# Optimization experiments

Measured on AMD Instinct MI355X. Metric: run time of the kernel, lower is better.

The kernel has to match this reference:

```python
import jax, jax.numpy as jnp
import numpy as np

H = 12  # num_attention_heads

def setup_inputs() -> dict:
    key = jax.random.key(0)
    ks = jax.random.split(key, 6)
    B, S, D = 2, 2048, 768
    sc = 0.02
    return {
        "hidden_states": jax.random.normal(ks[0], (B, S, D), jnp.float32),
        "Wqr": jax.random.normal(ks[1], (D, D), jnp.float32) * sc,
        "Wqi": jax.random.normal(ks[2], (D, D), jnp.float32) * sc,
        "Wkr": jax.random.normal(ks[3], (D, D), jnp.float32) * sc,
        "Wki": jax.random.normal(ks[4], (D, D), jnp.float32) * sc,
        "Wv": jax.random.normal(ks[5], (D, D), jnp.float32) * sc,
    }

def _heads(x, B, S):
    # [B,S,D] -> [B,H,S,Dh]
    return x.reshape(B, S, H, -1).transpose(0, 2, 1, 3)

def reference(hidden_states, Wqr, Wqi, Wkr, Wki, Wv):
    B, S, D = hidden_states.shape
    Dh = D // H
    x = hidden_states  # real input; imag part is zero
    # complex projections with zero imag input: q = (x@Wqr.T) + i (x@Wqi.T), same for k
    qr = _heads(x @ Wqr.T, B, S)
    qi = _heads(x @ Wqi.T, B, S)
    kr = _heads(x @ Wkr.T, B, S)
    ki = _heads(x @ Wki.T, B, S)
    v = _heads(x @ Wv.T, B, S)
    scale = 1.0 / jnp.sqrt(jnp.float32(Dh))
    # complex QK^H in real arithmetic: s = q @ conj(k)^T
    sr = (jnp.einsum('bhqd,bhkd->bhqk', qr, kr) +
          jnp.einsum('bhqd,bhkd->bhqk', qi, ki)) * scale
    si = (jnp.einsum('bhqd,bhkd->bhqk', qi, kr) -
          jnp.einsum('bhqd,bhkd->bhqk', qr, ki)) * scale
    scores = jnp.sqrt(sr * sr + si * si)  # 'magnitude' variant
    probs = jax.nn.softmax(scores, axis=-1)
    ctx = jnp.einsum('bhqk,bhkd->bhqd', probs, v)
    return ctx.transpose(0, 2, 1, 3).reshape(B, S, D)
```

## Files before the change

kernel.cpp:

```cpp
#include <hip/hip_runtime.h>
#include <cstdint>

typedef short bf16x8 __attribute__((ext_vector_type(8)));
typedef float f32x4 __attribute__((ext_vector_type(4)));

#define MFMA16(a, b, c) __builtin_amdgcn_mfma_f32_16x16x32_bf16((a), (b), (c), 0, 0, 0)

__device__ __forceinline__ void gl16(const unsigned short* g, unsigned short* l) {
  __builtin_amdgcn_global_load_lds(
      (const __attribute__((address_space(1))) unsigned int*)g,
      (__attribute__((address_space(3))) unsigned int*)l, 16, 0, 0);
}

__device__ __forceinline__ unsigned short f2b(float f) {
  union { float f; unsigned int u; } x; x.f = f;
  unsigned int r = x.u + 0x7fffu + ((x.u >> 16) & 1u);
  return (unsigned short)(r >> 16);
}

__device__ __forceinline__ unsigned int pack2(float lo, float hi) {
  union { float f; unsigned int u; } a, b;
  a.f = lo; b.f = hi;
  return ((a.u + 0x8000u) >> 16) | ((b.u + 0x8000u) & 0xffff0000u);
}

#define NB 2
#define NS 2048
#define ND 768
#define NH 12
#define DHD 64
#define MTOK 4096

#define OFF_XB 0
#define OFF_WB 3145728
#define OFF_QK 6094848
#define OFF_VT 18677760

__global__ void cvt_kernel(const float* __restrict__ src,
                           unsigned short* __restrict__ dst, int n4, float scale) {
  int i = blockIdx.x * blockDim.x + threadIdx.x;
  if (i >= n4) return;
  float4 v = ((const float4*)src)[i];
  ushort4 o;
  o.x = f2b(v.x * scale); o.y = f2b(v.y * scale);
  o.z = f2b(v.z * scale); o.w = f2b(v.w * scale);
  ((ushort4*)dst)[i] = o;
}

__global__ void wcvt_kernel(const float* __restrict__ s0, const float* __restrict__ s1,
                            const float* __restrict__ s2, const float* __restrict__ s3,
                            const float* __restrict__ s4, unsigned short* __restrict__ dst,
                            float qs) {
  const int bz = blockIdx.x / 576;
  const int i = (blockIdx.x % 576) * 256 + threadIdx.x;
  const float* src = bz == 0 ? s0 : bz == 1 ? s1 : bz == 2 ? s2 : bz == 3 ? s3 : s4;
  const float scale = bz < 2 ? qs : 1.0f;
  float4 v = ((const float4*)src)[i];
  ushort4 o;
  o.x = f2b(v.x * scale); o.y = f2b(v.y * scale);
  o.z = f2b(v.z * scale); o.w = f2b(v.w * scale);
  ((ushort4*)(dst + bz * 589824))[i] = o;
}

__global__ __launch_bounds__(256) void proj_kernel(
    const unsigned short* __restrict__ Xb, const unsigned short* __restrict__ Wb,
    unsigned short* __restrict__ QK, unsigned short* __restrict__ Vt) {
  __shared__ __align__(16) unsigned short S[32768];

  const int lin = blockIdx.x + 6 * (blockIdx.y + 5 * blockIdx.z);
  const int sb = (lin & 7) * 120 + (lin >> 3);
  const int n0 = (sb % 6) * 128;
  const int rem = sb / 6;
  const int z = rem % 5;
  const int m0 = (rem / 5) * 128;

  const unsigned short* Wz = Wb + z * 589824;
  const int tid = threadIdx.x;
  const int lane = tid & 63;
  const int w = tid >> 6;
  const int wm = (w >> 1) * 64;
  const int wn = (w & 1) * 64;
  const int col = lane & 15, quad = lane >> 4;
  const int c7 = col & 7;

  const int lr = lane >> 3;
  const int lc = (lane & 7) ^ (lr & 7);
  const unsigned short* gX = Xb + (m0 + w * 32 + lr) * ND + lc * 8;
  const unsigned short* gW = Wz + (n0 + w * 32 + lr) * ND + lc * 8;
  unsigned short* lX = S + (w * 32) * 64;
  unsigned short* lW = S + 16384 + (w * 32) * 64;

  f32x4 acc[4][4] = {};

#pragma unroll
  for (int i = 0; i < 4; i++) {
    gl16(gX + i * (8 * ND), lX + i * 512);
    gl16(gW + i * (8 * ND), lW + i * 512);
  }
  __syncthreads();

  int cur = 0;
  for (int kk = 0; kk < 12; kk++) {
    if (kk < 11) {
      const int k0n = (kk + 1) * 64;
      unsigned short* dX = lX + ((cur ^ 1) * 8192);
      unsigned short* dW = lW + ((cur ^ 1) * 8192);
#pragma unroll
      for (int i = 0; i < 4; i++) {
        gl16(gX + i * (8 * ND) + k0n, dX + i * 512);
        gl16(gW + i * (8 * ND) + k0n, dW + i * 512);
      }
    }
    const unsigned short* Xc = S + cur * 8192;
    const unsigned short* Wc = S + 16384 + cur * 8192;
#pragma unroll
    for (int ks = 0; ks < 2; ks++) {
      bf16x8 af[4], bw[4];
#pragma unroll
      for (int t = 0; t < 4; t++) {
        const int fo = (((ks * 4 + quad) ^ c7) * 8);
        af[t] = *(const bf16x8*)(Xc + (wm + t * 16 + col) * 64 + fo);
        bw[t] = *(const bf16x8*)(Wc + (wn + t * 16 + col) * 64 + fo);
      }
#pragma unroll
      for (int mt = 0; mt < 4; mt++)
#pragma unroll
        for (int nt = 0; nt < 4; nt++)
          acc[mt][nt] = MFMA16(af[mt], bw[nt], acc[mt][nt]);
    }
    __syncthreads();
    cur ^= 1;
  }

  unsigned short* T = S;

  if (z < 4) {
#pragma unroll
    for (int mt = 0; mt < 4; mt++) {
      int rl = wm + mt * 16 + quad * 4;
#pragma unroll
      for (int nt = 0; nt < 4; nt++) {
        int cl = wn + nt * 16 + col;
#pragma unroll
        for (int r = 0; r < 4; r++) T[(rl + r) * 136 + cl] = f2b(acc[mt][nt][r]);
      }
    }
    __syncthreads();
    unsigned short* out = QK + z * (MTOK * ND);
    const int rr = tid >> 4;
    const int cc = (tid & 15) * 8;
#pragma unroll
    for (int p = 0; p < 8; p++) {
      int row = p * 16 + rr;
      uint4 v = *(const uint4*)(T + row * 136 + cc);
      *(uint4*)(out + (m0 + row) * ND + n0 + cc) = v;
    }
  } else {
#pragma unroll
    for (int mt = 0; mt < 4; mt++) {
      int rl = wm + mt * 16 + quad * 4;
#pragma unroll
      for (int nt = 0; nt < 4; nt++) {
        int cl = wn + nt * 16 + col;
        ushort4 pk;
        pk.x = f2b(acc[mt][nt][0]);
        pk.y = f2b(acc[mt][nt][1]);
        pk.z = f2b(acc[mt][nt][2]);
        pk.w = f2b(acc[mt][nt][3]);
        *(ushort4*)(T + cl * 136 + rl) = pk;
      }
    }
    __syncthreads();
    const int rr = tid >> 4;
    const int cc = (tid & 15) * 8;
    const int b = m0 >> 11;
    const int s_base = m0 & 2047;
#pragma unroll
    for (int p = 0; p < 8; p++) {
      int dhl = p * 16 + rr;
      int c = n0 + dhl;
      int h = c >> 6, dh = c & 63;
      uint4 v = *(const uint4*)(T + dhl * 136 + cc);
      *(uint4*)(Vt + (((b * NH + h) * DHD + dh) * NS + s_base + cc)) = v;
    }
  }
}

__global__ __launch_bounds__(256) void attn_kernel(
    const unsigned short* __restrict__ QK, const unsigned short* __restrict__ Vt,
    float* __restrict__ outp) {
  __shared__ __align__(16) unsigned short Krs[4096];
  __shared__ __align__(16) unsigned short Kis[4096];
  __shared__ __align__(16) unsigned short Vts[8192];
  __shared__ __align__(16) unsigned short Ps[4096];

  const int lin = blockIdx.x + 32 * (blockIdx.y + 12 * blockIdx.z);
  const int sb = (lin & 7) * 96 + (lin >> 3);
  const int qt = sb & 31;
  const int h = (sb >> 5) % 12;
  const int b = sb / 384;
  const int tid = threadIdx.x, lane = tid & 63, w = tid >> 6;
  const int col = lane & 15, quad = lane >> 4;
  const int c7 = col & 7;
  const int jb = quad ^ c7;
  const int f0 = jb * 8, f1 = (jb ^ 4) * 8;

  const unsigned short* Qr = QK;
  const unsigned short* Qi = QK + MTOK * ND;
  const unsigned short* Krp = QK + 2 * MTOK * ND;
  const unsigned short* Kip = QK + 3 * MTOK * ND;

  const int q_tok = b * NS + qt * 64 + w * 16 + col;
  const int qoff = q_tok * ND + h * DHD;

  bf16x8 qrf[2], qif[2], qrn[2];
#pragma unroll
  for (int kk = 0; kk < 2; kk++) {
    qrf[kk] = *(const bf16x8*)(Qr + qoff + kk * 32 + quad * 8);
    qif[kk] = *(const bf16x8*)(Qi + qoff + kk * 32 + quad * 8);
    qrn[kk] = qrf[kk] ^ (short)0x8000;
  }

  const int lr = lane >> 3;
  const int lc = (lane & 7) ^ (lr & 7);
  const unsigned short* gKr = Krp + (b * NS + w * 8 + lr) * ND + h * DHD + lc * 8;
  const unsigned short* gKi = Kip + (b * NS + w * 8 + lr) * ND + h * DHD + lc * 8;
  const unsigned short* gV = Vt + (b * NH + h) * (DHD * NS) + (w * 8 + lr) * NS + lc * 8;
  const int st = (w * 8) * 64;

  unsigned short* PsW = Ps + w * 1024;

  f32x4 o[4] = {};
  float lrow = 0.f;

  gl16(gKr, Krs + st);
  gl16(gKr + 32 * ND, Krs + st + 2048);
  gl16(gKi, Kis + st);
  gl16(gKi + 32 * ND, Kis + st + 2048);
  gl16(gV, Vts + st);
  gl16(gV + 32 * NS, Vts + st + 2048);
  gKr += 64 * ND;
  gKi += 64 * ND;
  gV += 64;

  int vb = 0;
  for (int kt = 0; kt < 32; kt++) {
    __syncthreads();

#pragma unroll
    for (int mt = 0; mt < 4; mt++) {
      f32x4 sr = {}, si = {};
      const int rowb = (mt * 16 + col) * 64;
      bf16x8 kr0 = *(const bf16x8*)(Krs + rowb + f0);
      bf16x8 ki0 = *(const bf16x8*)(Kis + rowb + f0);
      bf16x8 kr1 = *(const bf16x8*)(Krs + rowb + f1);
      bf16x8 ki1 = *(const bf16x8*)(Kis + rowb + f1);
      sr = MFMA16(kr0, qrf[0], sr);
      sr = MFMA16(ki0, qif[0], sr);
      si = MFMA16(kr0, qif[0], si);
      si = MFMA16(ki0, qrn[0], si);
      sr = MFMA16(kr1, qrf[1], sr);
      sr = MFMA16(ki1, qif[1], sr);
      si = MFMA16(kr1, qif[1], si);
      si = MFMA16(ki1, qrn[1], si);

      float e0, e1, e2, e3;
      {
        float m0f = __builtin_amdgcn_sqrtf(sr[0] * sr[0] + si[0] * si[0]);
        float m1f = __builtin_amdgcn_sqrtf(sr[1] * sr[1] + si[1] * si[1]);
        float m2f = __builtin_amdgcn_sqrtf(sr[2] * sr[2] + si[2] * si[2]);
        float m3f = __builtin_amdgcn_sqrtf(sr[3] * sr[3] + si[3] * si[3]);
        e0 = __builtin_amdgcn_exp2f(m0f);
        e1 = __builtin_amdgcn_exp2f(m1f);
        e2 = __builtin_amdgcn_exp2f(m2f);
        e3 = __builtin_amdgcn_exp2f(m3f);
      }
      lrow += (e0 + e1) + (e2 + e3);
      uint2 pk;
      pk.x = pack2(e0, e1);
      pk.y = pack2(e2, e3);
      *(uint2*)(PsW + col * 64 + (((mt * 2 + (quad >> 1)) ^ c7) * 8) + (quad & 1) * 4) = pk;
    }

    __syncthreads();

    if (kt < 31) {
      const int nb = (vb ^ 1) * 4096;
      gl16(gKr, Krs + st);
      gl16(gKr + 32 * ND, Krs + st + 2048);
      gl16(gKi, Kis + st);
      gl16(gKi + 32 * ND, Kis + st + 2048);
      gl16(gV, Vts + nb + st);
      gl16(gV + 32 * NS, Vts + nb + st + 2048);
      gKr += 64 * ND;
      gKi += 64 * ND;
      gV += 64;
    }

    const unsigned short* Vc = Vts + vb * 4096;
    bf16x8 pb0 = *(const bf16x8*)(PsW + col * 64 + f0);
    bf16x8 pb1 = *(const bf16x8*)(PsW + col * 64 + f1);
#pragma unroll
    for (int dt = 0; dt < 4; dt++) {
      const int rowv = (dt * 16 + col) * 64;
      bf16x8 va0 = *(const bf16x8*)(Vc + rowv + f0);
      bf16x8 va1 = *(const bf16x8*)(Vc + rowv + f1);
      o[dt] = MFMA16(va0, pb0, o[dt]);
      o[dt] = MFMA16(va1, pb1, o[dt]);
    }
    vb ^= 1;
  }

  lrow += __shfl_xor(lrow, 16);
  lrow += __shfl_xor(lrow, 32);
  float inv_l = 1.0f / lrow;
  float* op = outp + (size_t)q_tok * ND + h * DHD;
#pragma unroll
  for (int dt = 0; dt < 4; dt++) {
    float4 v;
    v.x = o[dt][0] * inv_l;
    v.y = o[dt][1] * inv_l;
    v.z = o[dt][2] * inv_l;
    v.w = o[dt][3] * inv_l;
    *(float4*)(op + dt * 16 + quad * 4) = v;
  }
}

extern "C" void kernel_launch(void* const* d_in, const int* in_sizes, int n_in,
                              void* d_out, int out_size, void* d_ws, size_t ws_size,
                              hipStream_t stream) {
  const float* X = (const float*)d_in[0];
  unsigned short* ws = (unsigned short*)d_ws;
  unsigned short* Xb = ws + OFF_XB;
  unsigned short* Wb = ws + OFF_WB;
  unsigned short* QK = ws + OFF_QK;
  unsigned short* Vt = ws + OFF_VT;

  const float QSCALE = 0.125f * 1.44269504088896f;

  cvt_kernel<<<3072, 256, 0, stream>>>(X, Xb, 786432, 1.0f);
  wcvt_kernel<<<2880, 256, 0, stream>>>((const float*)d_in[1], (const float*)d_in[2],
                                        (const float*)d_in[3], (const float*)d_in[4],
                                        (const float*)d_in[5], Wb, QSCALE);

  proj_kernel<<<dim3(6, 5, 32), 256, 0, stream>>>(Xb, Wb, QK, Vt);
  attn_kernel<<<dim3(32, 12, 2), 256, 0, stream>>>(QK, Vt, (float*)d_out);
}
```

Measured before the change: 185.7 us.

## Halve projection K-tile to shrink LDS, prefetch V earlier, add MFMA priority hints

The projection GEMM now stages K-slices of 32 instead of 64 with a 4-way XOR swizzle. That cuts its shared memory from 64KB to about 34KB, which can raise occupancy, at the cost of twice as many loop iterations and barriers. In the attention kernel, the V tile prefetch for the next step is issued at the top of the iteration instead of after the softmax barrier, so it overlaps with the score computation. s_setprio hints are placed around the MFMA blocks in both kernels to favour the matrix-issuing waves.

```diff
diff --git a/kernel.cpp b/kernel.cpp
--- a/kernel.cpp
+++ b/kernel.cpp
@@ -65,7 +65,7 @@
 __global__ __launch_bounds__(256) void proj_kernel(
     const unsigned short* __restrict__ Xb, const unsigned short* __restrict__ Wb,
     unsigned short* __restrict__ QK, unsigned short* __restrict__ Vt) {
-  __shared__ __align__(16) unsigned short S[32768];
+  __shared__ __align__(16) unsigned short S[17408];
 
   const int lin = blockIdx.x + 6 * (blockIdx.y + 5 * blockIdx.z);
   const int sb = (lin & 7) * 120 + (lin >> 3);
@@ -81,53 +81,48 @@
   const int wm = (w >> 1) * 64;
   const int wn = (w & 1) * 64;
   const int col = lane & 15, quad = lane >> 4;
-  const int c7 = col & 7;
-
-  const int lr = lane >> 3;
-  const int lc = (lane & 7) ^ (lr & 7);
+
+  const int lr = lane >> 2;
+  const int lc = (lane & 3) ^ (lr & 3);
   const unsigned short* gX = Xb + (m0 + w * 32 + lr) * ND + lc * 8;
   const unsigned short* gW = Wz + (n0 + w * 32 + lr) * ND + lc * 8;
-  unsigned short* lX = S + (w * 32) * 64;
-  unsigned short* lW = S + 16384 + (w * 32) * 64;
+  const int stg = (w * 32) * 32;
 
   f32x4 acc[4][4] = {};
 
-#pragma unroll
-  for (int i = 0; i < 4; i++) {
-    gl16(gX + i * (8 * ND), lX + i * 512);
-    gl16(gW + i * (8 * ND), lW + i * 512);
-  }
+  gl16(gX, S + stg);
+  gl16(gX + 16 * ND, S + stg + 512);
+  gl16(gW, S + 8192 + stg);
+  gl16(gW + 16 * ND, S + 8192 + stg + 512);
   __syncthreads();
 
   int cur = 0;
-  for (int kk = 0; kk < 12; kk++) {
-    if (kk < 11) {
-      const int k0n = (kk + 1) * 64;
-      unsigned short* dX = lX + ((cur ^ 1) * 8192);
-      unsigned short* dW = lW + ((cur ^ 1) * 8192);
-#pragma unroll
-      for (int i = 0; i < 4; i++) {
-        gl16(gX + i * (8 * ND) + k0n, dX + i * 512);
-        gl16(gW + i * (8 * ND) + k0n, dW + i * 512);
-      }
-    }
-    const unsigned short* Xc = S + cur * 8192;
-    const unsigned short* Wc = S + 16384 + cur * 8192;
-#pragma unroll
-    for (int ks = 0; ks < 2; ks++) {
-      bf16x8 af[4], bw[4];
-#pragma unroll
-      for (int t = 0; t < 4; t++) {
-        const int fo = (((ks * 4 + quad) ^ c7) * 8);
-        af[t] = *(const bf16x8*)(Xc + (wm + t * 16 + col) * 64 + fo);
-        bw[t] = *(const bf16x8*)(Wc + (wn + t * 16 + col) * 64 + fo);
-      }
-#pragma unroll
-      for (int mt = 0; mt < 4; mt++)
-#pragma unroll
-        for (int nt = 0; nt < 4; nt++)
-          acc[mt][nt] = MFMA16(af[mt], bw[nt], acc[mt][nt]);
-    }
+  const int foA = (quad ^ (col & 3)) * 8;
+  for (int kk = 0; kk < 24; kk++) {
+    if (kk < 23) {
+      const int k0n = (kk + 1) * 32;
+      unsigned short* dX = S + ((cur ^ 1) * 4096) + stg;
+      unsigned short* dW = S + 8192 + ((cur ^ 1) * 4096) + stg;
+      gl16(gX + k0n, dX);
+      gl16(gX + 16 * ND + k0n, dX + 512);
+      gl16(gW + k0n, dW);
+      gl16(gW + 16 * ND + k0n, dW + 512);
+    }
+    const unsigned short* Xc = S + cur * 4096;
+    const unsigned short* Wc = S + 8192 + cur * 4096;
+    bf16x8 af[4], bw[4];
+#pragma unroll
+    for (int t = 0; t < 4; t++) {
+      af[t] = *(const bf16x8*)(Xc + (wm + t * 16 + col) * 32 + foA);
+      bw[t] = *(const bf16x8*)(Wc + (wn + t * 16 + col) * 32 + foA);
+    }
+    __builtin_amdgcn_s_setprio(1);
+#pragma unroll
+    for (int mt = 0; mt < 4; mt++)
+#pragma unroll
+      for (int nt = 0; nt < 4; nt++)
+        acc[mt][nt] = MFMA16(af[mt], bw[nt], acc[mt][nt]);
+    __builtin_amdgcn_s_setprio(0);
     __syncthreads();
     cur ^= 1;
   }
@@ -247,6 +242,13 @@
   for (int kt = 0; kt < 32; kt++) {
     __syncthreads();
 
+    if (kt < 31) {
+      const int nb = (vb ^ 1) * 4096;
+      gl16(gV, Vts + nb + st);
+      gl16(gV + 32 * NS, Vts + nb + st + 2048);
+      gV += 64;
+    }
+
 #pragma unroll
     for (int mt = 0; mt < 4; mt++) {
       f32x4 sr = {}, si = {};
@@ -255,6 +257,7 @@
       bf16x8 ki0 = *(const bf16x8*)(Kis + rowb + f0);
       bf16x8 kr1 = *(const bf16x8*)(Krs + rowb + f1);
       bf16x8 ki1 = *(const bf16x8*)(Kis + rowb + f1);
+      __builtin_amdgcn_s_setprio(1);
       sr = MFMA16(kr0, qrf[0], sr);
       sr = MFMA16(ki0, qif[0], sr);
       si = MFMA16(kr0, qif[0], si);
@@ -263,6 +266,7 @@
       sr = MFMA16(ki1, qif[1], sr);
       si = MFMA16(kr1, qif[1], si);
       si = MFMA16(ki1, qrn[1], si);
+      __builtin_amdgcn_s_setprio(0);
 
       float e0, e1, e2, e3;
       {
@@ -285,21 +289,18 @@
     __syncthreads();
 
     if (kt < 31) {
-      const int nb = (vb ^ 1) * 4096;
       gl16(gKr, Krs + st);
       gl16(gKr + 32 * ND, Krs + st + 2048);
       gl16(gKi, Kis + st);
       gl16(gKi + 32 * ND, Kis + st + 2048);
-      gl16(gV, Vts + nb + st);
-      gl16(gV + 32 * NS, Vts + nb + st + 2048);
       gKr += 64 * ND;
       gKi += 64 * ND;
-      gV += 64;
     }
 
     const unsigned short* Vc = Vts + vb * 4096;
     bf16x8 pb0 = *(const bf16x8*)(PsW + col * 64 + f0);
     bf16x8 pb1 = *(const bf16x8*)(PsW + col * 64 + f1);
+    __builtin_amdgcn_s_setprio(1);
 #pragma unroll
     for (int dt = 0; dt < 4; dt++) {
       const int rowv = (dt * 16 + col) * 64;
@@ -308,6 +309,7 @@
       o[dt] = MFMA16(va0, pb0, o[dt]);
       o[dt] = MFMA16(va1, pb1, o[dt]);
     }
+    __builtin_amdgcn_s_setprio(0);
     vb ^= 1;
   }
 
```

After: 206.4 us. +11.1%, slower.

## Enlarge projection GEMM tiles to 256x256 with 512-thread blocks

Applied to the files above, without the earlier changes.

The projection GEMM moves from 128x128 tiles on 256 threads (960 blocks) to 256x256 tiles on 512 threads (240 blocks). Each wave now computes a 128x64 sub-tile with 8x4 MFMA accumulators. This raises operand reuse per LDS load and cuts global traffic per output. The epilogue is split into two staged halves so the 128KB of LDS can be reused. In exchange, 240 blocks may underfill the 256 CUs, and the larger accumulator count raises register pressure and lowers occupancy.

```diff
diff --git a/kernel.cpp b/kernel.cpp
--- a/kernel.cpp
+++ b/kernel.cpp
@@ -62,40 +62,39 @@
   ((ushort4*)(dst + bz * 589824))[i] = o;
 }
 
-__global__ __launch_bounds__(256) void proj_kernel(
+__global__ __launch_bounds__(512) void proj_kernel(
     const unsigned short* __restrict__ Xb, const unsigned short* __restrict__ Wb,
     unsigned short* __restrict__ QK, unsigned short* __restrict__ Vt) {
-  __shared__ __align__(16) unsigned short S[32768];
-
-  const int lin = blockIdx.x + 6 * (blockIdx.y + 5 * blockIdx.z);
-  const int sb = (lin & 7) * 120 + (lin >> 3);
-  const int n0 = (sb % 6) * 128;
-  const int rem = sb / 6;
-  const int z = rem % 5;
-  const int m0 = (rem / 5) * 128;
+  __shared__ __align__(16) unsigned short S[65536];
+
+  const int lin = blockIdx.x;
+  const int sb = (lin & 7) * 30 + (lin >> 3);
+  const int z = sb / 48;
+  const int rem = sb % 48;
+  const int m0 = (rem / 3) * 256;
+  const int n0 = (rem % 3) * 256;
 
   const unsigned short* Wz = Wb + z * 589824;
   const int tid = threadIdx.x;
   const int lane = tid & 63;
   const int w = tid >> 6;
-  const int wm = (w >> 1) * 64;
-  const int wn = (w & 1) * 64;
+  const int wm = (w >> 2) * 128;
+  const int wn = (w & 3) * 64;
   const int col = lane & 15, quad = lane >> 4;
   const int c7 = col & 7;
 
   const int lr = lane >> 3;
   const int lc = (lane & 7) ^ (lr & 7);
-  const unsigned short* gX = Xb + (m0 + w * 32 + lr) * ND + lc * 8;
-  const unsigned short* gW = Wz + (n0 + w * 32 + lr) * ND + lc * 8;
-  unsigned short* lX = S + (w * 32) * 64;
-  unsigned short* lW = S + 16384 + (w * 32) * 64;
-
-  f32x4 acc[4][4] = {};
+  const unsigned short* gX = Xb + (m0 + w * 8 + lr) * ND + lc * 8;
+  const unsigned short* gW = Wz + (n0 + w * 8 + lr) * ND + lc * 8;
+  const int stg = (w * 8) * 64;
+
+  f32x4 acc[8][4] = {};
 
 #pragma unroll
   for (int i = 0; i < 4; i++) {
-    gl16(gX + i * (8 * ND), lX + i * 512);
-    gl16(gW + i * (8 * ND), lW + i * 512);
+    gl16(gX + i * (64 * ND), S + stg + i * 4096);
+    gl16(gW + i * (64 * ND), S + 32768 + stg + i * 4096);
   }
   __syncthreads();
 
@@ -103,27 +102,28 @@
   for (int kk = 0; kk < 12; kk++) {
     if (kk < 11) {
       const int k0n = (kk + 1) * 64;
-      unsigned short* dX = lX + ((cur ^ 1) * 8192);
-      unsigned short* dW = lW + ((cur ^ 1) * 8192);
+      unsigned short* dA = S + ((cur ^ 1) * 16384) + stg;
+      unsigned short* dB = S + 32768 + ((cur ^ 1) * 16384) + stg;
 #pragma unroll
       for (int i = 0; i < 4; i++) {
-        gl16(gX + i * (8 * ND) + k0n, dX + i * 512);
-        gl16(gW + i * (8 * ND) + k0n, dW + i * 512);
-      }
-    }
-    const unsigned short* Xc = S + cur * 8192;
-    const unsigned short* Wc = S + 16384 + cur * 8192;
+        gl16(gX + i * (64 * ND) + k0n, dA + i * 4096);
+        gl16(gW + i * (64 * ND) + k0n, dB + i * 4096);
+      }
+    }
+    const unsigned short* Ac = S + cur * 16384;
+    const unsigned short* Bc = S + 32768 + cur * 16384;
 #pragma unroll
     for (int ks = 0; ks < 2; ks++) {
-      bf16x8 af[4], bw[4];
-#pragma unroll
-      for (int t = 0; t < 4; t++) {
-        const int fo = (((ks * 4 + quad) ^ c7) * 8);
-        af[t] = *(const bf16x8*)(Xc + (wm + t * 16 + col) * 64 + fo);
-        bw[t] = *(const bf16x8*)(Wc + (wn + t * 16 + col) * 64 + fo);
-      }
-#pragma unroll
-      for (int mt = 0; mt < 4; mt++)
+      const int fo = (((ks * 4 + quad) ^ c7) * 8);
+      bf16x8 af[8], bw[4];
+#pragma unroll
+      for (int t = 0; t < 8; t++)
+        af[t] = *(const bf16x8*)(Ac + (wm + t * 16 + col) * 64 + fo);
+#pragma unroll
+      for (int u = 0; u < 4; u++)
+        bw[u] = *(const bf16x8*)(Bc + (wn + u * 16 + col) * 64 + fo);
+#pragma unroll
+      for (int mt = 0; mt < 8; mt++)
 #pragma unroll
         for (int nt = 0; nt < 4; nt++)
           acc[mt][nt] = MFMA16(af[mt], bw[nt], acc[mt][nt]);
@@ -135,53 +135,68 @@
   unsigned short* T = S;
 
   if (z < 4) {
-#pragma unroll
-    for (int mt = 0; mt < 4; mt++) {
-      int rl = wm + mt * 16 + quad * 4;
-#pragma unroll
-      for (int nt = 0; nt < 4; nt++) {
-        int cl = wn + nt * 16 + col;
-#pragma unroll
-        for (int r = 0; r < 4; r++) T[(rl + r) * 136 + cl] = f2b(acc[mt][nt][r]);
-      }
-    }
-    __syncthreads();
     unsigned short* out = QK + z * (MTOK * ND);
-    const int rr = tid >> 4;
-    const int cc = (tid & 15) * 8;
-#pragma unroll
-    for (int p = 0; p < 8; p++) {
-      int row = p * 16 + rr;
-      uint4 v = *(const uint4*)(T + row * 136 + cc);
-      *(uint4*)(out + (m0 + row) * ND + n0 + cc) = v;
+    const int wrow = w >> 2;
+#pragma unroll
+    for (int half = 0; half < 2; half++) {
+      __syncthreads();
+      if (wrow == half) {
+#pragma unroll
+        for (int mt = 0; mt < 8; mt++) {
+          int rl = mt * 16 + quad * 4;
+#pragma unroll
+          for (int nt = 0; nt < 4; nt++) {
+            int cl = wn + nt * 16 + col;
+#pragma unroll
+            for (int r = 0; r < 4; r++) T[(rl + r) * 264 + cl] = f2b(acc[mt][nt][r]);
+          }
+        }
+      }
+      __syncthreads();
+#pragma unroll
+      for (int p = 0; p < 8; p++) {
+        int ci = p * 512 + tid;
+        int row = ci >> 5;
+        int c8 = (ci & 31) * 8;
+        uint4 v = *(const uint4*)(T + row * 264 + c8);
+        *(uint4*)(out + (m0 + half * 128 + row) * ND + n0 + c8) = v;
+      }
     }
   } else {
-#pragma unroll
-    for (int mt = 0; mt < 4; mt++) {
-      int rl = wm + mt * 16 + quad * 4;
-#pragma unroll
-      for (int nt = 0; nt < 4; nt++) {
-        int cl = wn + nt * 16 + col;
-        ushort4 pk;
-        pk.x = f2b(acc[mt][nt][0]);
-        pk.y = f2b(acc[mt][nt][1]);
-        pk.z = f2b(acc[mt][nt][2]);
-        pk.w = f2b(acc[mt][nt][3]);
-        *(ushort4*)(T + cl * 136 + rl) = pk;
-      }
-    }
-    __syncthreads();
-    const int rr = tid >> 4;
-    const int cc = (tid & 15) * 8;
     const int b = m0 >> 11;
     const int s_base = m0 & 2047;
-#pragma unroll
-    for (int p = 0; p < 8; p++) {
-      int dhl = p * 16 + rr;
-      int c = n0 + dhl;
-      int h = c >> 6, dh = c & 63;
-      uint4 v = *(const uint4*)(T + dhl * 136 + cc);
-      *(uint4*)(Vt + (((b * NH + h) * DHD + dh) * NS + s_base + cc)) = v;
+    const int wcolh = (w & 3) >> 1;
+#pragma unroll
+    for (int half = 0; half < 2; half++) {
+      __syncthreads();
+      if (wcolh == half) {
+        int clb = wn - half * 128;
+#pragma unroll
+        for (int mt = 0; mt < 8; mt++) {
+          int rl = wm + mt * 16 + quad * 4;
+#pragma unroll
+          for (int nt = 0; nt < 4; nt++) {
+            int cl = clb + nt * 16 + col;
+            ushort4 pk;
+            pk.x = f2b(acc[mt][nt][0]);
+            pk.y = f2b(acc[mt][nt][1]);
+            pk.z = f2b(acc[mt][nt][2]);
+            pk.w = f2b(acc[mt][nt][3]);
+            *(ushort4*)(T + cl * 264 + rl) = pk;
+          }
+        }
+      }
+      __syncthreads();
+#pragma unroll
+      for (int p = 0; p < 8; p++) {
+        int ci = p * 512 + tid;
+        int dhl = ci >> 5;
+        int s8 = (ci & 31) * 8;
+        int c = n0 + half * 128 + dhl;
+        int h = c >> 6, dh = c & 63;
+        uint4 v = *(const uint4*)(T + dhl * 264 + s8);
+        *(uint4*)(Vt + ((b * NH + h) * DHD + dh) * NS + s_base + s8) = v;
+      }
     }
   }
 }
@@ -343,6 +358,6 @@
                                         (const float*)d_in[3], (const float*)d_in[4],
                                         (const float*)d_in[5], Wb, QSCALE);
 
-  proj_kernel<<<dim3(6, 5, 32), 256, 0, stream>>>(Xb, Wb, QK, Vt);
+  proj_kernel<<<240, 512, 0, stream>>>(Xb, Wb, QK, Vt);
   attn_kernel<<<dim3(32, 12, 2), 256, 0, stream>>>(QK, Vt, (float*)d_out);
 }
```

New measurement: 183.5 us. About the same (-1.2%).
